# Kernel optimization log

Measured on AMD Instinct MI355X. Metric: run time of the kernel, lower is better.

The kernel has to match this reference:

```python
import jax, jax.numpy as jnp
import numpy as np

N_COMPONENTS = 64

def setup_inputs() -> dict:
    key = jax.random.key(0)
    x = jax.random.normal(key, (16, 128, 128, 128), dtype=jnp.float32)
    return {"x": x}

def reference(x):
    B = x.shape[0]
    C = x.shape[-1]
    flat = x.reshape(B, -1, C)                      # [B, N, C], N = H*W
    n = flat.shape[1]
    mean = jnp.mean(flat, axis=1, keepdims=True)    # [B, 1, C]
    centered = flat - mean                          # [B, N, C]
    cov = jnp.einsum('bnc,bnd->bcd', centered, centered) / jnp.float32(n - 1)  # [B, C, C]
    eigvals, eigvecs = jnp.linalg.eigh(cov)         # ascending eigenvalues
    idx = jnp.argsort(eigvals, axis=-1)[:, ::-1]    # descending order
    # gather eigenvector columns in descending-eigenvalue order
    top = jnp.take_along_axis(eigvecs, idx[:, None, :], axis=-1)[:, :, :N_COMPONENTS]  # [B, C, K]
    projected = jnp.einsum('bnc,bck->bnk', centered, top)  # [B, N, K]
    return projected.reshape(x.shape[:-1] + (N_COMPONENTS,))
```

## Files before the change

kernel.cpp:

```cpp
#include <hip/hip_runtime.h>

#define NC 128
#define KTOP 64
#define SMLSIZ 25
#define EPSF 5.9604645e-8f
#define SAFMINF 1.17549435e-38f
#define LDQ 129
#define THREADS 512

#define TBASEF 15400960
#define F_A    0
#define F_B    262144
#define F_Q    524288
#define F_Q2   786432
#define F_SM   1052672
#define F_VECS 1314816


__device__ __forceinline__ float slapy2f(float x, float y) {
  float xa = fabsf(x), ya = fabsf(y);
  float w = fmaxf(xa, ya), z = fminf(xa, ya);
  if (z == 0.f) return w;
  float r = z / w;
  return w * sqrtf(1.f + r * r);
}

__device__ __forceinline__ void slartgf(float f, float g, float* c, float* s, float* r) {
  if (g == 0.f) { *c = 1.f; *s = 0.f; *r = f; }
  else if (f == 0.f) { *c = 0.f; *s = (g >= 0.f) ? 1.f : -1.f; *r = fabsf(g); }
  else {
    float d_ = sqrtf(f * f + g * g);
    *c = fabsf(f) / d_;
    *r = (f >= 0.f) ? d_ : -d_;
    *s = g / (*r);
  }
}

__device__ void slaev2f(float a, float b, float c,
                        float* rt1, float* rt2, float* cs1, float* sn1) {
  float sm = a + c, df = a - c, adf = fabsf(df), tb = b + b, ab = fabsf(tb);
  float acmx, acmn;
  if (fabsf(a) > fabsf(c)) { acmx = a; acmn = c; } else { acmx = c; acmn = a; }
  float rt;
  if (adf > ab) { float t = ab / adf; rt = adf * sqrtf(1.f + t * t); }
  else if (adf < ab) { float t = adf / ab; rt = ab * sqrtf(1.f + t * t); }
  else rt = ab * sqrtf(2.f);
  int sgn1;
  if (sm < 0.f) { *rt1 = 0.5f * (sm - rt); sgn1 = -1; *rt2 = (acmx / (*rt1)) * acmn - (b / (*rt1)) * b; }
  else if (sm > 0.f) { *rt1 = 0.5f * (sm + rt); sgn1 = 1; *rt2 = (acmx / (*rt1)) * acmn - (b / (*rt1)) * b; }
  else { *rt1 = 0.5f * rt; *rt2 = -0.5f * rt; sgn1 = 1; }
  float cs; int sgn2;
  if (df >= 0.f) { cs = df + rt; sgn2 = 1; } else { cs = df - rt; sgn2 = -1; }
  float acs = fabsf(cs);
  if (acs > ab) {
    float ct = -tb / cs;
    *sn1 = 1.f / sqrtf(1.f + ct * ct);
    *cs1 = ct * (*sn1);
  } else {
    if (ab == 0.f) { *cs1 = 1.f; *sn1 = 0.f; }
    else { float tn = -cs / tb; *cs1 = 1.f / sqrtf(1.f + tn * tn); *sn1 = tn * (*cs1); }
  }
  if (sgn1 == sgn2) { float tn = *cs1; *cs1 = -(*sn1); *sn1 = tn; }
}

#define SDD(i) __shfl(dr, (i))
#define SEE(i) __shfl(er, (i))
__device__ void steqr_reg(float* d, float* e, int n, float* zb, int ldz, int lane) {
  const float eps = EPSF;
  const float eps2 = eps * eps;
  const float safmin = SAFMINF;
  for (int j = 0; j < n; j++)
    for (int i = lane; i < n; i += 64) zb[j * ldz + i] = (i == j) ? 1.f : 0.f;
  if (n <= 1) return;
  float dr = (lane < n) ? d[lane] : 0.f;
  float er = (lane < n - 1) ? e[lane] : 0.f;
  float cwr = 0.f, swr = 0.f;
  int nmaxit = n * 30, jtot = 0;
  int l1 = 1;
  while (true) {
    if (l1 > n) break;
    if (l1 > 1) er = (lane == l1 - 2) ? 0.f : er;
    int m;
    {
      int mm_;
      for (mm_ = l1; mm_ <= n - 1; mm_++) {
        float tst = fabsf(SEE(mm_ - 1));
        if (tst == 0.f) break;
        if (tst <= (sqrtf(fabsf(SDD(mm_ - 1))) * sqrtf(fabsf(SDD(mm_)))) * eps) {
          er = (lane == mm_ - 1) ? 0.f : er;
          break;
        }
      }
      m = mm_;
    }
    int l = l1, lsv = l, lend = m, lendsv = lend;
    l1 = m + 1;
    if (lend == l) continue;
    float anorm = 0.f;
    for (int i = l; i <= lend; i++) anorm = fmaxf(anorm, fabsf(SDD(i - 1)));
    for (int i = l; i <= lend - 1; i++) anorm = fmaxf(anorm, fabsf(SEE(i - 1)));
    if (anorm == 0.f) continue;
    if (fabsf(SDD(lend - 1)) < fabsf(SDD(l - 1))) { lend = lsv; l = lendsv; }
    if (lend > l) {
      while (true) {
        int m2;
        {
          int i;
          for (i = l; i <= lend - 1; i++) {
            float tst = fabsf(SEE(i - 1)); tst = tst * tst;
            if (tst <= (eps2 * fabsf(SDD(i - 1))) * fabsf(SDD(i)) + safmin) break;
          }
          m2 = i;
        }
        if (m2 < lend) er = (lane == m2 - 1) ? 0.f : er;
        float p = SDD(l - 1);
        if (m2 == l) { dr = (lane == l - 1) ? p : dr; l++; if (l <= lend) continue; else break; }
        if (m2 == l + 1) {
          float rt1, rt2, c_, s_;
          slaev2f(SDD(l - 1), SEE(l - 1), SDD(l), &rt1, &rt2, &c_, &s_);
          for (int i = lane; i < n; i += 64) {
            float t1 = zb[l * ldz + i];
            float t0 = zb[(l - 1) * ldz + i];
            zb[l * ldz + i] = c_ * t1 - s_ * t0;
            zb[(l - 1) * ldz + i] = s_ * t1 + c_ * t0;
          }
          dr = (lane == l - 1) ? rt1 : dr;
          dr = (lane == l) ? rt2 : dr;
          er = (lane == l - 1) ? 0.f : er;
          l += 2; if (l <= lend) continue; else break;
        }
        if (jtot == nmaxit) break;
        jtot++;
        float g = (SDD(l) - p) / (2.f * SEE(l - 1));
        float r = slapy2f(g, 1.f);
        g = SDD(m2 - 1) - p + SEE(l - 1) / (g + copysignf(r, g));
        float s_ = 1.f, c_ = 1.f; p = 0.f;
        for (int i = m2 - 1; i >= l; i--) {
          float ee = SEE(i - 1);
          float f = s_ * ee, b2 = c_ * ee;
          float cc, ss, rr;
          slartgf(g, f, &cc, &ss, &rr);
          c_ = cc; s_ = ss;
          if (i != m2 - 1) er = (lane == i) ? rr : er;
          g = SDD(i) - p;
          rr = (SDD(i - 1) - g) * s_ + 2.f * c_ * b2;
          p = s_ * rr;
          dr = (lane == i) ? (g + p) : dr;
          g = c_ * rr - b2;
          cwr = (lane == (i - l)) ? c_ : cwr;
          swr = (lane == (i - l)) ? (-s_) : swr;
        }
        int mm2 = m2 - l + 1;
        for (int jj = mm2 - 2; jj >= 0; jj--) {
          float ct_ = __shfl(cwr, jj), st_ = __shfl(swr, jj);
          int colj = l - 1 + jj;
          for (int i = lane; i < n; i += 64) {
            float t1 = zb[(colj + 1) * ldz + i];
            float t0 = zb[colj * ldz + i];
            zb[(colj + 1) * ldz + i] = ct_ * t1 - st_ * t0;
            zb[colj * ldz + i] = st_ * t1 + ct_ * t0;
          }
        }
        {
          float nv = SDD(l - 1) - p;
          dr = (lane == l - 1) ? nv : dr;
          er = (lane == l - 1) ? g : er;
        }
      }
    } else {
      while (true) {
        int m2;
        {
          int i;
          for (i = l; i >= lend + 1; i--) {
            float tst = fabsf(SEE(i - 2)); tst = tst * tst;
            if (tst <= (eps2 * fabsf(SDD(i - 1))) * fabsf(SDD(i - 2)) + safmin) break;
          }
          m2 = i;
        }
        if (m2 > lend) er = (lane == m2 - 2) ? 0.f : er;
        float p = SDD(l - 1);
        if (m2 == l) { dr = (lane == l - 1) ? p : dr; l--; if (l >= lend) continue; else break; }
        if (m2 == l - 1) {
          float rt1, rt2, c_, s_;
          slaev2f(SDD(l - 2), SEE(l - 2), SDD(l - 1), &rt1, &rt2, &c_, &s_);
          for (int i = lane; i < n; i += 64) {
            float t1 = zb[(l - 1) * ldz + i];
            float t0 = zb[(l - 2) * ldz + i];
            zb[(l - 1) * ldz + i] = c_ * t1 - s_ * t0;
            zb[(l - 2) * ldz + i] = s_ * t1 + c_ * t0;
          }
          dr = (lane == l - 2) ? rt1 : dr;
          dr = (lane == l - 1) ? rt2 : dr;
          er = (lane == l - 2) ? 0.f : er;
          l -= 2; if (l >= lend) continue; else break;
        }
        if (jtot == nmaxit) break;
        jtot++;
        float g = (SDD(l - 2) - p) / (2.f * SEE(l - 2));
        float r = slapy2f(g, 1.f);
        g = SDD(m2 - 1) - p + SEE(l - 2) / (g + copysignf(r, g));
        float s_ = 1.f, c_ = 1.f; p = 0.f;
        for (int i = m2; i <= l - 1; i++) {
          float ee = SEE(i - 1);
          float f = s_ * ee, b2 = c_ * ee;
          float cc, ss, rr;
          slartgf(g, f, &cc, &ss, &rr);
          c_ = cc; s_ = ss;
          if (i != m2) er = (lane == i - 2) ? rr : er;
          g = SDD(i - 1) - p;
          rr = (SDD(i) - g) * s_ + 2.f * c_ * b2;
          p = s_ * rr;
          dr = (lane == i - 1) ? (g + p) : dr;
          g = c_ * rr - b2;
          cwr = (lane == (i - m2)) ? c_ : cwr;
          swr = (lane == (i - m2)) ? s_ : swr;
        }
        int mm2 = l - m2 + 1;
        for (int jj = 0; jj <= mm2 - 2; jj++) {
          float ct_ = __shfl(cwr, jj), st_ = __shfl(swr, jj);
          int colj = m2 - 1 + jj;
          for (int i = lane; i < n; i += 64) {
            float t1 = zb[(colj + 1) * ldz + i];
            float t0 = zb[colj * ldz + i];
            zb[(colj + 1) * ldz + i] = ct_ * t1 - st_ * t0;
            zb[colj * ldz + i] = st_ * t1 + ct_ * t0;
          }
        }
        {
          float nv = SDD(l - 1) - p;
          dr = (lane == l - 1) ? nv : dr;
          er = (lane == l - 2) ? g : er;
        }
      }
    }
  }
  for (int ii = 2; ii <= n; ii++) {
    int i = ii - 1, k = i;
    float p = SDD(i - 1);
    for (int j = ii; j <= n; j++) {
      float dj = SDD(j - 1);
      if (dj < p) { k = j; p = dj; }
    }
    if (k != i) {
      float old = SDD(i - 1);
      dr = (lane == k - 1) ? old : dr;
      dr = (lane == i - 1) ? p : dr;
      for (int r = lane; r < n; r += 64) {
        float t5 = zb[(i - 1) * ldz + r];
        zb[(i - 1) * ldz + r] = zb[(k - 1) * ldz + r];
        zb[(k - 1) * ldz + r] = t5;
      }
    }
  }
  if (lane < n) d[lane] = dr;
  if (lane < n - 1) e[lane] = er;
}


__device__ void laed1_multi(float* d, float* e, float* Qm, float* Q2b, float* Smb,
                            float* zv, float* dl, float* wv, float* wg, float* pvf,
                            float* dvf, int* srcx, int* dsrc, int* iq,
                            int goff, const int* iwps, int p0, int G,
                            int tid, int* shi, float* shdf,
                            double* sdl, double* spv, int* defcnt) {
  int Tg = THREADS / G;
  int g = tid / Tg, gtid = tid - g * Tg;
  int pg = 2 * (p0 + g);
  int prev = (pg == 0) ? 0 : iwps[pg - 1];
  int off = goff + prev;
  int n = iwps[pg + 1] - prev;
  int n1 = (pg == 0) ? iwps[0] : (n / 2);
  int n2 = n - n1;
  float rho_in = e[off + n1 - 1];
  float* dg = d + off;
  float* zvg = zv + off;  float* dlg = dl + off;  float* wvg = wv + off;
  float* wgg = wg + off;  float* pvfg = pvf + off; float* dvfg = dvf + off;
  int* srcxg = srcx + off; int* dsrcg = dsrc + off; int* iqg = iq + off;
  double* sdlg = sdl + off; double* spvg = spv + off;
  float* Q2g = Q2b + (size_t)off * 128;
  float* Smg = Smb + (size_t)off * 128 + off;

  for (int t = gtid; t < n1; t += Tg) zvg[t] = Qm[(off + t) * LDQ + off + n1 - 1];
  for (int t = gtid; t < n2; t += Tg) zvg[n1 + t] = Qm[(off + n1 + t) * LDQ + off + n1];
  __syncthreads();
  if (gtid == 0) {
    float rho = rho_in;
    if (rho < 0.f) for (int t = n1; t < n; t++) zvg[t] = -zvg[t];
    float tsc = 1.0f / sqrtf(2.0f);
    for (int t = 0; t < n; t++) zvg[t] *= tsc;
    rho = fabsf(2.0f * rho);
    {
      int i = 0, j = n1, p = 0;
      while (i < n1 && j < n) {
        if (dg[i] <= dg[j]) srcxg[p++] = i++; else srcxg[p++] = j++;
      }
      while (i < n1) srcxg[p++] = i++;
      while (j < n) srcxg[p++] = j++;
    }
    int imax = 0, jmax = 0;
    for (int t = 1; t < n; t++) if (fabsf(zvg[t]) > fabsf(zvg[imax])) imax = t;
    for (int t = 1; t < n; t++) if (fabsf(dg[t]) > fabsf(dg[jmax])) jmax = t;
    float tol = 8.0f * EPSF * fmaxf(fabsf(dg[jmax]), fabsf(zvg[imax]));
    int k = 0, nd = 0;
    if (rho * fabsf(zvg[imax]) <= tol) {
      for (int t = 0; t < n; t++) { dsrcg[nd] = srcxg[t]; dvfg[nd] = dg[srcxg[t]]; nd++; }
    } else {
      int pj = -1;
      for (int jj = 0; jj < n; jj++) {
        int nj = srcxg[jj];
        if (rho * fabsf(zvg[nj]) <= tol) {
          dsrcg[nd] = nj; dvfg[nd] = dg[nj]; nd++;
        } else if (pj < 0) {
          pj = nj;
        } else {
          float s_ = zvg[pj], c_ = zvg[nj];
          float tau_ = slapy2f(c_, s_);
          float t3 = dg[nj] - dg[pj];
          c_ /= tau_; s_ = -s_ / tau_;
          if (fabsf(t3 * c_ * s_) <= tol) {
            zvg[nj] = tau_; zvg[pj] = 0.f;
            for (int r = 0; r < n; r++) {
              float x_ = Qm[(off + pj) * LDQ + off + r];
              float y_ = Qm[(off + nj) * LDQ + off + r];
              Qm[(off + pj) * LDQ + off + r] = c_ * x_ + s_ * y_;
              Qm[(off + nj) * LDQ + off + r] = c_ * y_ - s_ * x_;
            }
            float dp = dg[pj], dn = dg[nj];
            dg[nj] = dp * s_ * s_ + dn * c_ * c_;
            dg[pj] = dp * c_ * c_ + dn * s_ * s_;
            dsrcg[nd] = pj; dvfg[nd] = dg[pj]; nd++;
            pj = nj;
          } else {
            dlg[k] = dg[pj]; wvg[k] = zvg[pj]; srcxg[k] = pj; k++;
            pj = nj;
          }
        }
      }
      if (pj >= 0) { dlg[k] = dg[pj]; wvg[k] = zvg[pj]; srcxg[k] = pj; k++; }
    }
    shi[200 + g] = k; shi[208 + g] = nd; shdf[8 + g] = rho;
    if (nd > 0) atomicAdd(defcnt, nd);
  }
  __syncthreads();
  int k = shi[200 + g], nd = shi[208 + g];
  float rho = shdf[8 + g];
  if (k > 1) {
    for (int t = gtid; t < k; t += Tg) {
      sdlg[t] = (double)dlg[t];
      spvg[t] = (double)rho * (double)wvg[t] * (double)wvg[t];
    }
  }
  __syncthreads();
  if (k > 1 && gtid < k) {
    int j = gtid;
    double lo = 0.0, hi;
    if (j == k - 1) {
      double sw2 = 0.0;
      for (int t = 0; t < k; t++) sw2 += spvg[t];
      hi = sw2;
      for (int g2 = 0; g2 < 8; g2++) {
        double f = 1.0;
        for (int t = 0; t < k; t++) f += spvg[t] / ((sdlg[t] - sdlg[j]) - hi);
        if (f >= 0.0) break;
        hi *= 2.0;
      }
    } else hi = sdlg[j + 1] - sdlg[j];
    double gap = hi;
    double x = 0.5 * (lo + hi);
    for (int it = 0; it < 60; it++) {
      double f = 1.0, fp = 0.0;
      for (int t = 0; t < k; t++) {
        double inv = 1.0 / ((sdlg[t] - sdlg[j]) - x);
        double u = spvg[t] * inv;
        f += u; fp += u * inv;
      }
      if (f < 0.0) lo = x; else hi = x;
      double xn = x - f / fp;
      if (!(xn > lo && xn < hi)) xn = 0.5 * (lo + hi);
      if (xn == x) break;
      x = xn;
    }
    double eta = x;
    if (eta <= 0.0) eta = gap * 1e-30;
    if (j < k - 1 && eta >= gap) eta = gap * (1.0 - 1e-15);
    dg[j] = (float)(sdlg[j] + eta);
    for (int t = 0; t < k; t++)
      Smg[t * 128 + j] = (float)((sdlg[t] - sdlg[j]) - eta);
  }
  __syncthreads();
  if (k > 1 && gtid < k) {
    int i = gtid;
    float acc = Smg[i * 128 + i];
    for (int j = 0; j < k; j++) {
      if (j == i) continue;
      acc *= Smg[i * 128 + j] / (dlg[i] - dlg[j]);
    }
    wgg[i] = copysignf(sqrtf(fmaxf(-acc, 0.f)), wvg[i]);
  }
  __syncthreads();
  if (k > 1 && gtid < k) {
    int j = gtid;
    float nrm2 = 0.f;
    for (int i = 0; i < k; i++) {
      float u = wgg[i] / Smg[i * 128 + j];
      Smg[i * 128 + j] = u;
      nrm2 += u * u;
    }
    float nrm = sqrtf(nrm2);
    for (int i = 0; i < k; i++) Smg[i * 128 + j] /= nrm;
  }
  __syncthreads();
  if (k > 1) {
    int j = gtid & 127, rg = gtid >> 7;
    int RG = Tg >> 7; if (RG < 1) RG = 1;
    if (j < k) {
      int chunk = (n + RG - 1) / RG;
      int rbeg = rg * chunk, rend = rbeg + chunk;
      if (rend > n) rend = n;
      int r0 = rbeg;
      for (; r0 + 8 <= rend; r0 += 8) {
        float a0 = 0.f, a1 = 0.f, a2 = 0.f, a3 = 0.f;
        float a4 = 0.f, a5 = 0.f, a6 = 0.f, a7 = 0.f;
        for (int i = 0; i < k; i++) {
          float s = Smg[i * 128 + j];
          const float* q = &Qm[(off + srcxg[i]) * LDQ + off + r0];
          a0 += q[0] * s; a1 += q[1] * s; a2 += q[2] * s; a3 += q[3] * s;
          a4 += q[4] * s; a5 += q[5] * s; a6 += q[6] * s; a7 += q[7] * s;
        }
        float* o = &Q2g[j * 128 + r0];
        o[0] = a0; o[1] = a1; o[2] = a2; o[3] = a3;
        o[4] = a4; o[5] = a5; o[6] = a6; o[7] = a7;
      }
      for (; r0 < rend; r0++) {
        float a = 0.f;
        for (int i = 0; i < k; i++)
          a += Qm[(off + srcxg[i]) * LDQ + off + r0] * Smg[i * 128 + j];
        Q2g[j * 128 + r0] = a;
      }
    }
  } else if (k == 1 && gtid == 0) {
    zvg[0] = dlg[0] + rho * (wvg[0] * wvg[0]);
    for (int r = 0; r < n; r++) Q2g[r] = Qm[(off + srcxg[0]) * LDQ + off + r];
  }
  __syncthreads();
  if (k > 1 && gtid < k) zvg[gtid] = dg[gtid];
  __syncthreads();
  for (int t2 = gtid; t2 < nd; t2 += Tg)
    for (int r = 0; r < n; r++) Q2g[(k + t2) * 128 + r] = Qm[(off + dsrcg[t2]) * LDQ + off + r];
  for (int j = gtid; j < n; j += Tg) pvfg[j] = (j < k) ? zvg[j] : dvfg[j - k];
  __syncthreads();
  for (int j = gtid; j < n; j += Tg) {
    float kj = pvfg[j];
    int r = 0;
    for (int i = 0; i < n; i++) {
      float ki = pvfg[i];
      if (ki < kj || (ki == kj && i < j)) r++;
    }
    iqg[r] = j;
  }
  __syncthreads();
  {
    int j = gtid & 127, rg = gtid >> 7;
    int RG = Tg >> 7; if (RG < 1) RG = 1;
    if (j < n) {
      int s2 = iqg[j];
      if (rg == 0) dg[j] = pvfg[s2];
      int chunk = (n + RG - 1) / RG;
      int rbeg = rg * chunk, rend = rbeg + chunk;
      if (rend > n) rend = n;
      for (int r = rbeg; r < rend; r++) Qm[(off + j) * LDQ + off + r] = Q2g[s2 * 128 + r];
    }
  }
  __syncthreads();
}

__device__ void laed0_f32(float* d, float* e, float* Qm, float* Q2, float* Sm,
                          float* zv, float* dl, float* wv, float* wg, float* pvf,
                          float* dvf, int* srcx, int* dsrc, int* iq, int* iwps,
                          int goff, int m, int tid, int* shi, float* shdf,
                          double* sdl, double* spv, int* defcnt) {
  if (tid == 0) {
    iwps[0] = m; int sp = 1;
    while (iwps[sp - 1] > SMLSIZ) {
      for (int j = sp - 1; j >= 0; j--) { iwps[2 * j + 1] = (iwps[j] + 1) / 2; iwps[2 * j] = iwps[j] / 2; }
      sp *= 2;
    }
    for (int j = 1; j < sp; j++) iwps[j] += iwps[j - 1];
    shi[134] = sp;
    for (int i = 0; i < sp - 1; i++) {
      int bnd = goff + iwps[i];
      d[bnd - 1] -= fabsf(e[bnd - 1]);
      d[bnd] -= fabsf(e[bnd - 1]);
    }
  }
  __syncthreads();
  int subpbs = shi[134];
  {
    int lw = tid >> 6;
    if (lw < subpbs) {
      int boff = goff + (lw == 0 ? 0 : iwps[lw - 1]);
      int bm = iwps[lw] - (lw == 0 ? 0 : iwps[lw - 1]);
      steqr_reg(d + boff, e + boff, bm, Qm + boff * LDQ + boff, LDQ, tid & 63);
    }
  }
  __syncthreads();
  int cur = subpbs;
  while (cur > 1) {
    int nm = cur >> 1;
    for (int p0 = 0; p0 < nm; ) {
      int G = (nm - p0 >= 4) ? 4 : ((nm - p0 >= 2) ? 2 : 1);
      laed1_multi(d, e, Qm, Q2, Sm, zv, dl, wv, wg, pvf, dvf, srcx, dsrc, iq,
                  goff, iwps, p0, G, tid, shi, shdf, sdl, spv, defcnt);
      p0 += G;
    }
    if (tid == 0) for (int t = 0; 2 * t + 1 < cur; t++) iwps[t] = iwps[2 * t + 1];
    __syncthreads();
    cur >>= 1;
  }
}


__global__ __launch_bounds__(THREADS) void eig_p1_kernel(const float* __restrict__ covB,
                                                         float* __restrict__ Aout,
                                                         float* __restrict__ vecs) {
  int b = blockIdx.x, tid = threadIdx.x;
  const float* Cg = covB + (size_t)b * 16384;
  float* Ag = Aout + (size_t)b * 16384;
  __shared__ float As[16384];
  __shared__ float sh_e[128], sh_tau[128], sh_pvf[128];
  __shared__ float redf[128];
  __shared__ float shdf[4];
  float* A = As; float* e = sh_e; float* tauv = sh_tau; float* pvf = sh_pvf;

  for (int idx = tid; idx < 16384; idx += THREADS) As[idx] = Cg[idx];
  if (tid < 128) { sh_e[tid] = 0.f; sh_tau[tid] = 0.f; }
  __syncthreads();

  for (int i1 = 1; i1 <= NC - 1; i1++) {
    int ii = i1 - 1;
    int mlen = NC - i1;
    float ps = 0.f;
    if (tid < 128) {
      for (int t = tid; t < mlen - 1; t += 128) {
        float v = A[ii * 128 + ii + 2 + t];
        ps += v * v;
      }
      redf[tid] = ps;
    }
    __syncthreads();
    if (tid < 64) {
      float a = redf[tid] + redf[tid + 64];
      a += __shfl_xor(a, 32); a += __shfl_xor(a, 16); a += __shfl_xor(a, 8);
      a += __shfl_xor(a, 4);  a += __shfl_xor(a, 2);  a += __shfl_xor(a, 1);
      if (tid == 0) {
        float xnorm = sqrtf(a);
        float alpha = A[ii * 128 + ii + 1];
        float taui, ei, scl;
        if (xnorm == 0.f) { taui = 0.f; ei = alpha; scl = 0.f; }
        else {
          float beta = -copysignf(slapy2f(alpha, xnorm), alpha);
          taui = (beta - alpha) / beta;
          scl = 1.f / (alpha - beta);
          ei = beta;
        }
        e[ii] = ei; tauv[ii] = taui; shdf[2] = scl;
      }
    }
    __syncthreads();
    float taui = tauv[ii];
    if (taui != 0.f) {
      float scl = shdf[2];
      for (int t = tid; t < mlen - 1; t += 128) A[ii * 128 + ii + 2 + t] *= scl;
      __syncthreads();
      for (int r = tid; r < mlen; r += 128) {
        float acc = 0.f;
        int row = ii + 1 + r;
        acc += A[(ii + 1) * 128 + row];
        for (int s = 1; s < mlen; s++) acc += A[(ii + 1 + s) * 128 + row] * A[ii * 128 + ii + 1 + s];
        pvf[r] = taui * acc;
      }
      __syncthreads();
      if (tid < 128) {
        float pd = 0.f;
        for (int t = tid; t < mlen; t += 128) {
          float vt = (t == 0) ? 1.f : A[ii * 128 + ii + 1 + t];
          pd += pvf[t] * vt;
        }
        redf[tid] = pd;
      }
      __syncthreads();
      if (tid < 64) {
        float a = redf[tid] + redf[tid + 64];
        a += __shfl_xor(a, 32); a += __shfl_xor(a, 16); a += __shfl_xor(a, 8);
        a += __shfl_xor(a, 4);  a += __shfl_xor(a, 2);  a += __shfl_xor(a, 1);
        if (tid == 0) shdf[3] = -0.5f * taui * a;
      }
      __syncthreads();
      float alpha2 = shdf[3];
      for (int t = tid; t < mlen; t += 128) {
        float vt = (t == 0) ? 1.f : A[ii * 128 + ii + 1 + t];
        pvf[t] += alpha2 * vt;
      }
      __syncthreads();
      if ((tid & 127) < mlen) {
        int r = tid & 127, g = tid >> 7;
        int chunk = (mlen + 3) >> 2;
        int cb = g * chunk, ce = cb + chunk;
        if (ce > mlen) ce = mlen;
        float vr = (r == 0) ? 1.f : A[ii * 128 + ii + 1 + r];
        float pr = pvf[r];
        for (int c2 = cb; c2 < ce; c2++) {
          float vc = (c2 == 0) ? 1.f : A[ii * 128 + ii + 1 + c2];
          A[(ii + 1 + c2) * 128 + (ii + 1 + r)] -= vr * pvf[c2] + pr * vc;
        }
      }
      __syncthreads();
    }
  }
  for (int idx = tid; idx < 16384; idx += THREADS) Ag[idx] = As[idx];
  if (tid < 128) {
    vecs[b * 128 + tid] = As[tid * 128 + tid];
    vecs[2048 + b * 128 + tid] = sh_e[tid];
    vecs[4096 + b * 128 + tid] = sh_tau[tid];
  }
}


__global__ __launch_bounds__(THREADS) void eig_p2_kernel(float* __restrict__ Qw,
                                                         float* Q2w, float* Sw,
                                                         float* vecs, int* defcnt) {
  int b = blockIdx.x, tid = threadIdx.x;
  float* Qg = Qw + (size_t)b * 16384;
  float* Q2 = Q2w + (size_t)b * 16640;
  float* Sm = Sw + (size_t)b * 16384;

  __shared__ float Qs[128 * LDQ];
  __shared__ float sh_d[128], sh_e[128], sh_zv[128], sh_dl[128];
  __shared__ float sh_wv[128], sh_wg[128], sh_pvf[128], sh_dvf[128];
  __shared__ int sh_iq[128], sh_srcx[128], sh_dsrc[128];
  __shared__ int iwps[64];
  __shared__ float shdf[16];
  __shared__ int shi[280];
  __shared__ double sdl[128];
  __shared__ double spv[128];

  float* Qm = Qs;
  float* d = sh_d; float* e = sh_e; float* zv = sh_zv;
  float* dl = sh_dl; float* wv = sh_wv; float* wg = sh_wg; float* pvf = sh_pvf;
  float* dvf = sh_dvf;
  int* iq = sh_iq; int* srcx = sh_srcx; int* dsrc = sh_dsrc;

  if (tid < 128) {
    sh_d[tid] = vecs[b * 128 + tid];
    sh_e[tid] = vecs[2048 + b * 128 + tid];
  }
  for (int idx = tid; idx < 16384; idx += THREADS) {
    int c = idx >> 7, r = idx & 127;
    Qs[c * LDQ + r] = (c == r) ? 1.f : 0.f;
  }
  __syncthreads();
  if (tid == 0) {
    int ns = 0, start = 0;
    while (start < NC) {
      int fin = start;
      while (fin < NC - 1) {
        float tiny = EPSF * sqrtf(fabsf(d[fin])) * sqrtf(fabsf(d[fin + 1]));
        if (fabsf(e[fin]) > tiny) fin++;
        else break;
      }
      shi[2 + 2 * ns] = start; shi[3 + 2 * ns] = fin - start + 1; ns++;
      start = fin + 1;
    }
    shi[0] = ns;
  }
  __syncthreads();
  int nsplit = shi[0];
  for (int sb = 0; sb < nsplit; sb++) {
    int goff = shi[2 + 2 * sb], m = shi[3 + 2 * sb];
    if (m == 1) continue;
    if (m <= SMLSIZ) {
      if (tid < 64) steqr_reg(d + goff, e + goff, m, Qm + goff * LDQ + goff, LDQ, tid);
      __syncthreads();
    } else {
      if (tid == 0) {
        float mx = 0.f;
        for (int i = 0; i < m; i++) mx = fmaxf(mx, fabsf(d[goff + i]));
        for (int i = 0; i < m - 1; i++) mx = fmaxf(mx, fabsf(e[goff + i]));
        shdf[0] = mx;
      }
      __syncthreads();
      float onrm = shdf[0];
      if (onrm != 0.f) {
        float mul = 1.f / onrm;
        for (int t = tid; t < m; t += 128) d[goff + t] *= mul;
        for (int t = tid; t < m - 1; t += 128) e[goff + t] *= mul;
        __syncthreads();
        laed0_f32(d, e, Qm, Q2, Sm, zv, dl, wv, wg, pvf, dvf, srcx, dsrc, iq,
                  iwps, goff, m, tid, shi, shdf, sdl, spv, defcnt);
        for (int t = tid; t < m; t += 128) d[goff + t] *= onrm;
        __syncthreads();
      }
    }
  }
  if (tid < 128) {
    float kj = d[tid];
    int r = 0;
    for (int i = 0; i < 128; i++) {
      float ki = d[i];
      if (ki < kj || (ki == kj && i < tid)) r++;
    }
    shi[140 + r] = tid;
    zv[r] = kj;
  }
  __syncthreads();
  if (tid < 128) d[tid] = zv[tid];
  __syncthreads();
  {
    int j = tid & 127, g = tid >> 7;
    int rbeg = g * 32, rend = rbeg + 32;
    int src = shi[140 + j];
    for (int r = rbeg; r < rend; r++) Q2[j * 128 + r] = Qm[src * LDQ + r];
  }
  __syncthreads();
  {
    int j = tid & 127, g = tid >> 7;
    int rbeg = g * 32, rend = rbeg + 32;
    for (int r = rbeg; r < rend; r++) Qm[j * LDQ + r] = Q2[j * 128 + r];
  }
  __syncthreads();
  for (int idx = tid; idx < 16384; idx += THREADS) {
    int c = idx >> 7, r = idx & 127;
    Qg[idx] = Qs[c * LDQ + r];
  }
  if (tid < 128) vecs[b * 128 + tid] = d[tid];
}


__global__ __launch_bounds__(THREADS) void eig_p3_kernel(const float* __restrict__ Ain,
                                                         const float* __restrict__ vecs,
                                                         float* __restrict__ Qw,
                                                         float* __restrict__ Vw) {
  int b = blockIdx.x, tid = threadIdx.x;
  const float* Ag = Ain + (size_t)b * 16384;
  float* Qg = Qw + (size_t)b * 16384;
  __shared__ float As[16384];
  __shared__ float Qs[128 * LDQ];
  __shared__ float sh_tau[128];
  float* A = As; float* Qm = Qs; float* tauv = sh_tau;

  for (int idx = tid; idx < 16384; idx += THREADS) As[idx] = Ag[idx];
  for (int idx = tid; idx < 16384; idx += THREADS) {
    int c = idx >> 7, r = idx & 127;
    Qs[c * LDQ + r] = Qg[idx];
  }
  if (tid < 128) sh_tau[tid] = vecs[4096 + b * 128 + tid];
  __syncthreads();

  for (int j1 = NC - 1; j1 >= 1; j1--) {
    int jj = j1 - 1;
    float tj = tauv[jj];
    if (tj != 0.f) {
      if (tid < NC) {
        int col = tid;
        float s = Qm[col * LDQ + jj + 1];
        for (int r = jj + 2; r < NC; r++) s += A[jj * 128 + r] * Qm[col * LDQ + r];
        s *= tj;
        Qm[col * LDQ + jj + 1] -= s;
        for (int r = jj + 2; r < NC; r++) Qm[col * LDQ + r] -= s * A[jj * 128 + r];
      }
    }
  }
  __syncthreads();

  for (int idx = tid; idx < NC * KTOP; idx += THREADS) {
    int c2 = idx / KTOP, kk = idx % KTOP;
    Vw[(size_t)b * (NC * KTOP) + idx] = Qm[(127 - kk) * LDQ + c2];
  }
  for (int idx = tid; idx < 16384; idx += THREADS) {
    int c = idx >> 7, r = idx & 127;
    Qg[idx] = Qs[c * LDQ + r];
  }
}


__global__ void zeroi_kernel(int* p) { p[0] = 0; p[1] = 0; }

__global__ __launch_bounds__(128) void diag_kernel(const float* __restrict__ covB,
                                                   const float* __restrict__ Qw,
                                                   const float* __restrict__ vecs,
                                                   const float* __restrict__ Vw, int* dcode) {
  int b = blockIdx.x, tid = threadIdx.x;
  const float* C = covB + (size_t)b * 16384;
  const float* Qm = Qw + (size_t)b * 16384;
  const float* d = vecs + b * 128;
  int flags = 0;
  double rmax = 0.0;
  for (int k = 64; k < 128; k++) {
    double lam = (double)d[k];
    double acc = 0.0;
    for (int j = 0; j < 128; j++) acc += (double)C[j * 128 + tid] * (double)Qm[k * 128 + j];
    acc -= lam * (double)Qm[k * 128 + tid];
    rmax = fmax(rmax, fabs(acc));
  }
  if (rmax > 1e-3) flags |= 1;
  double omax = 0.0;
  for (int p = tid; p < 64 * 64; p += 128) {
    int i = 64 + p / 64, j = 64 + p % 64;
    if (j < i) continue;
    double s = 0.0;
    for (int r = 0; r < 128; r++) s += (double)Qm[i * 128 + r] * (double)Qm[j * 128 + r];
    if (i == j) s -= 1.0;
    omax = fmax(omax, fabs(s));
  }
  if (omax > 1e-3) flags |= 2;
  if (tid < 127 && d[tid + 1] < d[tid] - 1e-5f) flags |= 4;
  for (int idx = tid; idx < 8192; idx += 128) {
    int c2 = idx / 64, kk = idx % 64;
    if (Vw[(size_t)b * 8192 + idx] != Qm[(127 - kk) * 128 + c2]) flags |= 8;
  }
  if (tid == 0) {
    for (int k = 64; k < 128; k++) if (!(d[k] > 0.2f && d[k] < 5.0f)) flags |= 16;
    float s = 0.f;
    for (int c = 0; c < 128; c++) { float v = Vw[(size_t)b * 8192 + c * 64]; s += v * v; }
    if (fabsf(s - 1.f) > 1e-2f) flags |= 32;
  }
  if (flags) atomicOr(dcode, flags);
}

__global__ void emit_kernel(const int* dcode, float* out) {
  int f = dcode[0];
  if (f) {
    int code = 1000;
    if (f & 1) code += 400;
    if (f & 2) code += 200;
    if (f & 4) code += 100;
    if (f & 8) code += 40;
    if (f & 16) code += 20;
    if (f & 32) code += 10;
    int nd = dcode[1]; if (nd > 9) nd = 9;
    code += nd;
    out[0] = (float)code;
  }
}


__global__ __launch_bounds__(128) void mean_np_kernel(const float* __restrict__ x,
                                                      float* __restrict__ mean32) {
  int b = blockIdx.x, c = threadIdx.x;
  const float* xb = x + (size_t)b * 2097152;
  float s = 0.0f;
#pragma unroll 16
  for (int n = 0; n < 16384; n++) s = __fadd_rn(s, xb[n * 128 + c]);
  mean32[b * 128 + c] = s / 16384.0f;
}

__global__ __launch_bounds__(256) void covnp_kernel(const float* __restrict__ x,
                                                    const float* __restrict__ mean32,
                                                    float* __restrict__ S) {
  int b = blockIdx.x;
  int p = blockIdx.y;
  int ti4, tj4;
  if (p < 4) { ti4 = 0; tj4 = p; }
  else if (p < 7) { ti4 = 1; tj4 = p - 3; }
  else if (p < 9) { ti4 = 2; tj4 = p - 5; }
  else { ti4 = 3; tj4 = 3; }
  int ti = ti4 * 32, tj = tj4 * 32;
  __shared__ float XI[32 * 66], XJ[32 * 66];
  int tid = threadIdx.x;
  int ci = 2 * (tid & 15), dj = 2 * (tid >> 4);
  float a00 = 0.f, a01 = 0.f, a10 = 0.f, a11 = 0.f;
  const float* xb = x + (size_t)b * 2097152;
  const float* mb = mean32 + b * 128;
  for (int n0 = 0; n0 < 16384; n0 += 64) {
    __syncthreads();
    for (int l = tid; l < 2048; l += 256) {
      int n = l >> 5, cc = l & 31;
      XI[cc * 66 + n] = __fsub_rn(xb[(n0 + n) * 128 + ti + cc], mb[ti + cc]);
      XJ[cc * 66 + n] = __fsub_rn(xb[(n0 + n) * 128 + tj + cc], mb[tj + cc]);
    }
    __syncthreads();
    const float2* pi0 = (const float2*)&XI[ci * 66];
    const float2* pi1 = (const float2*)&XI[(ci + 1) * 66];
    const float2* pj0 = (const float2*)&XJ[dj * 66];
    const float2* pj1 = (const float2*)&XJ[(dj + 1) * 66];
    for (int n2 = 0; n2 < 32; n2++) {
      float2 xi0 = pi0[n2], xi1 = pi1[n2], xj0 = pj0[n2], xj1 = pj1[n2];
      a00 = __fadd_rn(a00, __fmul_rn(xi0.x, xj0.x));
      a01 = __fadd_rn(a01, __fmul_rn(xi0.x, xj1.x));
      a10 = __fadd_rn(a10, __fmul_rn(xi1.x, xj0.x));
      a11 = __fadd_rn(a11, __fmul_rn(xi1.x, xj1.x));
      a00 = __fadd_rn(a00, __fmul_rn(xi0.y, xj0.y));
      a01 = __fadd_rn(a01, __fmul_rn(xi0.y, xj1.y));
      a10 = __fadd_rn(a10, __fmul_rn(xi1.y, xj0.y));
      a11 = __fadd_rn(a11, __fmul_rn(xi1.y, xj1.y));
    }
  }
  float* Sb = S + (size_t)b * 16384;
  int C = ti + ci, D = tj + dj;
  Sb[C * 128 + D] = a00;
  Sb[C * 128 + D + 1] = a01;
  Sb[(C + 1) * 128 + D] = a10;
  Sb[(C + 1) * 128 + D + 1] = a11;
}

__global__ void covfin_kernel(const float* __restrict__ A, float* __restrict__ B) {
  int i = blockIdx.x * 256 + threadIdx.x;
  if (i < 262144) {
    int w = i & 16383;
    int base = i - w;
    int r = w >> 7, c = w & 127;
    int src = ((r >> 5) > (c >> 5)) ? (base + c * 128 + r) : i;
    B[i] = A[src] / 16383.0f;
  }
}


__global__ __launch_bounds__(256) void proj_kernel(const float* __restrict__ x, const float* __restrict__ V,
                                                   const float* __restrict__ mean32, float* __restrict__ out) {
  __shared__ float Vs[128 * 64];
  __shared__ float Xs[64 * 128];
  __shared__ float ms[128];
  int b = blockIdx.x, t = blockIdx.y, tid = threadIdx.x;
  const float* xb = x + (size_t)b * 2097152 + (size_t)t * 64 * 128;
  const float* vb = V + (size_t)b * 8192;
  if (tid < 128) ms[tid] = mean32[b * 128 + tid];
  __syncthreads();
  for (int i = tid; i < 2048; i += 256) ((float4*)Vs)[i] = ((const float4*)vb)[i];
  for (int i = tid; i < 2048; i += 256) {
    float4 xv = ((const float4*)xb)[i];
    int cv = (i & 31) * 4;
    xv.x -= ms[cv]; xv.y -= ms[cv + 1]; xv.z -= ms[cv + 2]; xv.w -= ms[cv + 3];
    ((float4*)Xs)[i] = xv;
  }
  __syncthreads();
  int kk = tid & 63, w = tid >> 6;
  float acc[16];
#pragma unroll
  for (int r = 0; r < 16; r++) acc[r] = 0.f;
  for (int c4 = 0; c4 < 32; c4++) {
    float v0 = Vs[(c4 * 4 + 0) * 64 + kk];
    float v1 = Vs[(c4 * 4 + 1) * 64 + kk];
    float v2 = Vs[(c4 * 4 + 2) * 64 + kk];
    float v3 = Vs[(c4 * 4 + 3) * 64 + kk];
#pragma unroll
    for (int r = 0; r < 16; r++) {
      const float4 xv = ((const float4*)Xs)[(w * 16 + r) * 32 + c4];
      acc[r] += xv.x * v0 + xv.y * v1 + xv.z * v2 + xv.w * v3;
    }
  }
  float* ob = out + (size_t)b * 1048576 + (size_t)t * 4096;
#pragma unroll
  for (int r = 0; r < 16; r++) ob[(w * 16 + r) * 64 + kk] = acc[r];
}


extern "C" void kernel_launch(void* const* d_in, const int* in_sizes, int n_in,
                              void* d_out, int out_size, void* d_ws, size_t ws_size,
                              hipStream_t stream) {
  (void)in_sizes; (void)n_in; (void)out_size; (void)ws_size;
  const float* x = (const float*)d_in[0];
  float* out = (float*)d_out;
  float* T = out + TBASEF;
  float* Af   = T + F_A;
  float* Bf   = T + F_B;
  float* Qf   = T + F_Q;
  float* Q2f  = T + F_Q2;
  float* Smf  = T + F_SM;
  float* vecsf = T + F_VECS;
  float* Vw = (float*)d_ws;
  float* mean32 = Vw + 131072;
  int* dcode = (int*)(mean32 + 2048);

  zeroi_kernel<<<dim3(1), dim3(1), 0, stream>>>(dcode);
  mean_np_kernel<<<dim3(16), dim3(128), 0, stream>>>(x, mean32);
  covnp_kernel<<<dim3(16, 10), dim3(256), 0, stream>>>(x, mean32, Af);
  covfin_kernel<<<dim3(1024), dim3(256), 0, stream>>>(Af, Bf);
  eig_p1_kernel<<<dim3(16), dim3(THREADS), 0, stream>>>(Bf, Af, vecsf);
  eig_p2_kernel<<<dim3(16), dim3(THREADS), 0, stream>>>(Qf, Q2f, Smf, vecsf, dcode + 1);
  eig_p3_kernel<<<dim3(16), dim3(THREADS), 0, stream>>>(Af, vecsf, Qf, Vw);
  diag_kernel<<<dim3(16), dim3(128), 0, stream>>>(Bf, Qf, vecsf, Vw, dcode);
  proj_kernel<<<dim3(16, 256), dim3(256), 0, stream>>>(x, Vw, mean32, out);
  emit_kernel<<<dim3(1), dim3(1), 0, stream>>>(dcode, out);
}
```

Before: 4.776 ms.

## Split eigen merge into three kernels and keep secular matrix in LDS

The divide-and-conquer eigensolver stage is split into three launches: leaf QR solves, all merges except the last, and the final merge plus sort. Split metadata and norms are passed through the vecs workspace. The secular-equation matrix Sm moves from global memory to a padded LDS array (stride 129), removing global round-trips in the merge's inner loops. The cost is extra launches, Q reloads and stores between stages, and higher per-block LDS use. The mean kernel's unroll factor also rises from 16 to 64.

```diff
diff --git a/kernel.cpp b/kernel.cpp
--- a/kernel.cpp
+++ b/kernel.cpp
@@ -6,6 +6,7 @@
 #define EPSF 5.9604645e-8f
 #define SAFMINF 1.17549435e-38f
 #define LDQ 129
+#define LDS_SM 129
 #define THREADS 512
 
 #define TBASEF 15400960
@@ -13,7 +14,6 @@
 #define F_B    262144
 #define F_Q    524288
 #define F_Q2   786432
-#define F_SM   1052672
 #define F_VECS 1314816
 
 
@@ -279,7 +279,7 @@
   int* srcxg = srcx + off; int* dsrcg = dsrc + off; int* iqg = iq + off;
   double* sdlg = sdl + off; double* spvg = spv + off;
   float* Q2g = Q2b + (size_t)off * 128;
-  float* Smg = Smb + (size_t)off * 128 + off;
+  float* Smg = Smb + (size_t)off * LDS_SM + off;
 
   for (int t = gtid; t < n1; t += Tg) zvg[t] = Qm[(off + t) * LDQ + off + n1 - 1];
   for (int t = gtid; t < n2; t += Tg) zvg[n1 + t] = Qm[(off + n1 + t) * LDQ + off + n1];
@@ -386,15 +386,15 @@
     if (j < k - 1 && eta >= gap) eta = gap * (1.0 - 1e-15);
     dg[j] = (float)(sdlg[j] + eta);
     for (int t = 0; t < k; t++)
-      Smg[t * 128 + j] = (float)((sdlg[t] - sdlg[j]) - eta);
+      Smg[t * LDS_SM + j] = (float)((sdlg[t] - sdlg[j]) - eta);
   }
   __syncthreads();
   if (k > 1 && gtid < k) {
     int i = gtid;
-    float acc = Smg[i * 128 + i];
+    float acc = Smg[i * LDS_SM + i];
     for (int j = 0; j < k; j++) {
       if (j == i) continue;
-      acc *= Smg[i * 128 + j] / (dlg[i] - dlg[j]);
+      acc *= Smg[i * LDS_SM + j] / (dlg[i] - dlg[j]);
     }
     wgg[i] = copysignf(sqrtf(fmaxf(-acc, 0.f)), wvg[i]);
   }
@@ -403,12 +403,12 @@
     int j = gtid;
     float nrm2 = 0.f;
     for (int i = 0; i < k; i++) {
-      float u = wgg[i] / Smg[i * 128 + j];
-      Smg[i * 128 + j] = u;
+      float u = wgg[i] / Smg[i * LDS_SM + j];
+      Smg[i * LDS_SM + j] = u;
       nrm2 += u * u;
     }
     float nrm = sqrtf(nrm2);
-    for (int i = 0; i < k; i++) Smg[i * 128 + j] /= nrm;
+    for (int i = 0; i < k; i++) Smg[i * LDS_SM + j] /= nrm;
   }
   __syncthreads();
   if (k > 1) {
@@ -423,7 +423,7 @@
         float a0 = 0.f, a1 = 0.f, a2 = 0.f, a3 = 0.f;
         float a4 = 0.f, a5 = 0.f, a6 = 0.f, a7 = 0.f;
         for (int i = 0; i < k; i++) {
-          float s = Smg[i * 128 + j];
+          float s = Smg[i * LDS_SM + j];
           const float* q = &Qm[(off + srcxg[i]) * LDQ + off + r0];
           a0 += q[0] * s; a1 += q[1] * s; a2 += q[2] * s; a3 += q[3] * s;
           a4 += q[4] * s; a5 += q[5] * s; a6 += q[6] * s; a7 += q[7] * s;
@@ -435,7 +435,7 @@
       for (; r0 < rend; r0++) {
         float a = 0.f;
         for (int i = 0; i < k; i++)
-          a += Qm[(off + srcxg[i]) * LDQ + off + r0] * Smg[i * 128 + j];
+          a += Qm[(off + srcxg[i]) * LDQ + off + r0] * Smg[i * LDS_SM + j];
         Q2g[j * 128 + r0] = a;
       }
     }
@@ -473,51 +473,6 @@
     }
   }
   __syncthreads();
-}
-
-__device__ void laed0_f32(float* d, float* e, float* Qm, float* Q2, float* Sm,
-                          float* zv, float* dl, float* wv, float* wg, float* pvf,
-                          float* dvf, int* srcx, int* dsrc, int* iq, int* iwps,
-                          int goff, int m, int tid, int* shi, float* shdf,
-                          double* sdl, double* spv, int* defcnt) {
-  if (tid == 0) {
-    iwps[0] = m; int sp = 1;
-    while (iwps[sp - 1] > SMLSIZ) {
-      for (int j = sp - 1; j >= 0; j--) { iwps[2 * j + 1] = (iwps[j] + 1) / 2; iwps[2 * j] = iwps[j] / 2; }
-      sp *= 2;
-    }
-    for (int j = 1; j < sp; j++) iwps[j] += iwps[j - 1];
-    shi[134] = sp;
-    for (int i = 0; i < sp - 1; i++) {
-      int bnd = goff + iwps[i];
-      d[bnd - 1] -= fabsf(e[bnd - 1]);
-      d[bnd] -= fabsf(e[bnd - 1]);
-    }
-  }
-  __syncthreads();
-  int subpbs = shi[134];
-  {
-    int lw = tid >> 6;
-    if (lw < subpbs) {
-      int boff = goff + (lw == 0 ? 0 : iwps[lw - 1]);
-      int bm = iwps[lw] - (lw == 0 ? 0 : iwps[lw - 1]);
-      steqr_reg(d + boff, e + boff, bm, Qm + boff * LDQ + boff, LDQ, tid & 63);
-    }
-  }
-  __syncthreads();
-  int cur = subpbs;
-  while (cur > 1) {
-    int nm = cur >> 1;
-    for (int p0 = 0; p0 < nm; ) {
-      int G = (nm - p0 >= 4) ? 4 : ((nm - p0 >= 2) ? 2 : 1);
-      laed1_multi(d, e, Qm, Q2, Sm, zv, dl, wv, wg, pvf, dvf, srcx, dsrc, iq,
-                  goff, iwps, p0, G, tid, shi, shdf, sdl, spv, defcnt);
-      p0 += G;
-    }
-    if (tid == 0) for (int t = 0; 2 * t + 1 < cur; t++) iwps[t] = iwps[2 * t + 1];
-    __syncthreads();
-    cur >>= 1;
-  }
 }
 
 
@@ -627,15 +582,108 @@
 }
 
 
-__global__ __launch_bounds__(THREADS) void eig_p2_kernel(float* __restrict__ Qw,
-                                                         float* Q2w, float* Sw,
-                                                         float* vecs, int* defcnt) {
+__global__ __launch_bounds__(THREADS) void eig_p2a_kernel(float* __restrict__ Qw,
+                                                          float* __restrict__ vecs) {
+  int b = blockIdx.x, tid = threadIdx.x;
+  float* Qg = Qw + (size_t)b * 16384;
+  __shared__ float Qs[128 * LDQ];
+  __shared__ float sh_d[128], sh_e[128];
+  __shared__ int iwps[64];
+  __shared__ float shdf[16];
+  __shared__ int shi[280];
+  float* Qm = Qs; float* d = sh_d; float* e = sh_e;
+  int* meta = (int*)(vecs + 6144) + b * 320;
+  float* onrmv = vecs + 11264 + b * 128;
+
+  if (tid < 128) { sh_d[tid] = vecs[b * 128 + tid]; sh_e[tid] = vecs[2048 + b * 128 + tid]; }
+  for (int idx = tid; idx < 16384; idx += THREADS) {
+    int c = idx >> 7, r = idx & 127;
+    Qs[c * LDQ + r] = (c == r) ? 1.f : 0.f;
+  }
+  __syncthreads();
+  if (tid == 0) {
+    int ns = 0, start = 0;
+    while (start < NC) {
+      int fin = start;
+      while (fin < NC - 1) {
+        float tiny = EPSF * sqrtf(fabsf(d[fin])) * sqrtf(fabsf(d[fin + 1]));
+        if (fabsf(e[fin]) > tiny) fin++;
+        else break;
+      }
+      shi[2 + 2 * ns] = start; shi[3 + 2 * ns] = fin - start + 1; ns++;
+      start = fin + 1;
+    }
+    shi[0] = ns;
+    meta[0] = ns;
+    for (int s = 0; s < ns; s++) { meta[1 + 2 * s] = shi[2 + 2 * s]; meta[2 + 2 * s] = shi[3 + 2 * s]; }
+  }
+  __syncthreads();
+  int nsplit = shi[0];
+  for (int sb = 0; sb < nsplit; sb++) {
+    int goff = shi[2 + 2 * sb], m = shi[3 + 2 * sb];
+    if (m == 1) { if (tid == 0) onrmv[sb] = 0.f; continue; }
+    if (m <= SMLSIZ) {
+      if (tid == 0) onrmv[sb] = 0.f;
+      if (tid < 64) steqr_reg(d + goff, e + goff, m, Qm + goff * LDQ + goff, LDQ, tid);
+      __syncthreads();
+    } else {
+      if (tid == 0) {
+        float mx = 0.f;
+        for (int i = 0; i < m; i++) mx = fmaxf(mx, fabsf(d[goff + i]));
+        for (int i = 0; i < m - 1; i++) mx = fmaxf(mx, fabsf(e[goff + i]));
+        shdf[0] = mx;
+        onrmv[sb] = mx;
+      }
+      __syncthreads();
+      float onrm = shdf[0];
+      if (onrm != 0.f) {
+        float mul = 1.f / onrm;
+        for (int t = tid; t < m; t += 128) d[goff + t] *= mul;
+        for (int t = tid; t < m - 1; t += 128) e[goff + t] *= mul;
+        __syncthreads();
+        if (tid == 0) {
+          iwps[0] = m; int sp = 1;
+          while (iwps[sp - 1] > SMLSIZ) {
+            for (int j = sp - 1; j >= 0; j--) { iwps[2 * j + 1] = (iwps[j] + 1) / 2; iwps[2 * j] = iwps[j] / 2; }
+            sp *= 2;
+          }
+          for (int j = 1; j < sp; j++) iwps[j] += iwps[j - 1];
+          shi[134] = sp;
+          for (int i = 0; i < sp - 1; i++) {
+            int bnd = goff + iwps[i];
+            d[bnd - 1] -= fabsf(e[bnd - 1]);
+            d[bnd] -= fabsf(e[bnd - 1]);
+          }
+        }
+        __syncthreads();
+        int subpbs = shi[134];
+        {
+          int lw = tid >> 6;
+          if (lw < subpbs) {
+            int boff = goff + (lw == 0 ? 0 : iwps[lw - 1]);
+            int bm = iwps[lw] - (lw == 0 ? 0 : iwps[lw - 1]);
+            steqr_reg(d + boff, e + boff, bm, Qm + boff * LDQ + boff, LDQ, tid & 63);
+          }
+        }
+        __syncthreads();
+      }
+    }
+  }
+  if (tid < 128) { vecs[b * 128 + tid] = sh_d[tid]; vecs[2048 + b * 128 + tid] = sh_e[tid]; }
+  for (int idx = tid; idx < 16384; idx += THREADS) {
+    int c = idx >> 7, r = idx & 127;
+    Qg[idx] = Qs[c * LDQ + r];
+  }
+}
+
+
+__global__ __launch_bounds__(THREADS) void eig_p2b_kernel(float* __restrict__ Qw,
+                                                          float* Q2w, float* vecs, int* defcnt) {
   int b = blockIdx.x, tid = threadIdx.x;
   float* Qg = Qw + (size_t)b * 16384;
   float* Q2 = Q2w + (size_t)b * 16640;
-  float* Sm = Sw + (size_t)b * 16384;
-
   __shared__ float Qs[128 * LDQ];
+  __shared__ float Sms[128 * LDS_SM];
   __shared__ float sh_d[128], sh_e[128], sh_zv[128], sh_dl[128];
   __shared__ float sh_wv[128], sh_wg[128], sh_pvf[128], sh_dvf[128];
   __shared__ int sh_iq[128], sh_srcx[128], sh_dsrc[128];
@@ -644,64 +692,103 @@
   __shared__ int shi[280];
   __shared__ double sdl[128];
   __shared__ double spv[128];
-
   float* Qm = Qs;
-  float* d = sh_d; float* e = sh_e; float* zv = sh_zv;
-  float* dl = sh_dl; float* wv = sh_wv; float* wg = sh_wg; float* pvf = sh_pvf;
-  float* dvf = sh_dvf;
-  int* iq = sh_iq; int* srcx = sh_srcx; int* dsrc = sh_dsrc;
-
-  if (tid < 128) {
-    sh_d[tid] = vecs[b * 128 + tid];
-    sh_e[tid] = vecs[2048 + b * 128 + tid];
-  }
+  int* meta = (int*)(vecs + 6144) + b * 320;
+  float* onrmv = vecs + 11264 + b * 128;
+
+  if (tid < 128) { sh_d[tid] = vecs[b * 128 + tid]; sh_e[tid] = vecs[2048 + b * 128 + tid]; }
   for (int idx = tid; idx < 16384; idx += THREADS) {
     int c = idx >> 7, r = idx & 127;
-    Qs[c * LDQ + r] = (c == r) ? 1.f : 0.f;
-  }
-  __syncthreads();
-  if (tid == 0) {
-    int ns = 0, start = 0;
-    while (start < NC) {
-      int fin = start;
-      while (fin < NC - 1) {
-        float tiny = EPSF * sqrtf(fabsf(d[fin])) * sqrtf(fabsf(d[fin + 1]));
-        if (fabsf(e[fin]) > tiny) fin++;
-        else break;
-      }
-      shi[2 + 2 * ns] = start; shi[3 + 2 * ns] = fin - start + 1; ns++;
-      start = fin + 1;
-    }
-    shi[0] = ns;
-  }
-  __syncthreads();
-  int nsplit = shi[0];
+    Qs[c * LDQ + r] = Qg[idx];
+  }
+  __syncthreads();
+  int nsplit = meta[0];
   for (int sb = 0; sb < nsplit; sb++) {
-    int goff = shi[2 + 2 * sb], m = shi[3 + 2 * sb];
-    if (m == 1) continue;
-    if (m <= SMLSIZ) {
-      if (tid < 64) steqr_reg(d + goff, e + goff, m, Qm + goff * LDQ + goff, LDQ, tid);
+    int goff = meta[1 + 2 * sb], m = meta[2 + 2 * sb];
+    float onrm = onrmv[sb];
+    if (onrm == 0.f || m <= SMLSIZ) continue;
+    if (tid == 0) {
+      iwps[0] = m; int sp = 1;
+      while (iwps[sp - 1] > SMLSIZ) {
+        for (int j = sp - 1; j >= 0; j--) { iwps[2 * j + 1] = (iwps[j] + 1) / 2; iwps[2 * j] = iwps[j] / 2; }
+        sp *= 2;
+      }
+      for (int j = 1; j < sp; j++) iwps[j] += iwps[j - 1];
+      shi[134] = sp;
+    }
+    __syncthreads();
+    int cur = shi[134];
+    while (cur > 2) {
+      int nm = cur >> 1;
+      for (int p0 = 0; p0 < nm; ) {
+        int G = (nm - p0 >= 4) ? 4 : ((nm - p0 >= 2) ? 2 : 1);
+        laed1_multi(sh_d, sh_e, Qm, Q2, Sms, sh_zv, sh_dl, sh_wv, sh_wg, sh_pvf, sh_dvf,
+                    sh_srcx, sh_dsrc, sh_iq, goff, iwps, p0, G, tid, shi, shdf, sdl, spv, defcnt);
+        p0 += G;
+      }
+      if (tid == 0) for (int t = 0; 2 * t + 1 < cur; t++) iwps[t] = iwps[2 * t + 1];
       __syncthreads();
-    } else {
-      if (tid == 0) {
-        float mx = 0.f;
-        for (int i = 0; i < m; i++) mx = fmaxf(mx, fabsf(d[goff + i]));
-        for (int i = 0; i < m - 1; i++) mx = fmaxf(mx, fabsf(e[goff + i]));
-        shdf[0] = mx;
-      }
+      cur >>= 1;
+    }
+  }
+  if (tid < 128) vecs[b * 128 + tid] = sh_d[tid];
+  for (int idx = tid; idx < 16384; idx += THREADS) {
+    int c = idx >> 7, r = idx & 127;
+    Qg[idx] = Qs[c * LDQ + r];
+  }
+}
+
+
+__global__ __launch_bounds__(THREADS) void eig_p2c_kernel(float* __restrict__ Qw,
+                                                          float* Q2w, float* vecs, int* defcnt) {
+  int b = blockIdx.x, tid = threadIdx.x;
+  float* Qg = Qw + (size_t)b * 16384;
+  float* Q2 = Q2w + (size_t)b * 16640;
+  __shared__ float Qs[128 * LDQ];
+  __shared__ float Sms[128 * LDS_SM];
+  __shared__ float sh_d[128], sh_e[128], sh_zv[128], sh_dl[128];
+  __shared__ float sh_wv[128], sh_wg[128], sh_pvf[128], sh_dvf[128];
+  __shared__ int sh_iq[128], sh_srcx[128], sh_dsrc[128];
+  __shared__ int iwps[64];
+  __shared__ float shdf[16];
+  __shared__ int shi[280];
+  __shared__ double sdl[128];
+  __shared__ double spv[128];
+  float* Qm = Qs; float* d = sh_d; float* zv = sh_zv;
+  int* meta = (int*)(vecs + 6144) + b * 320;
+  float* onrmv = vecs + 11264 + b * 128;
+
+  if (tid < 128) { sh_d[tid] = vecs[b * 128 + tid]; sh_e[tid] = vecs[2048 + b * 128 + tid]; }
+  for (int idx = tid; idx < 16384; idx += THREADS) {
+    int c = idx >> 7, r = idx & 127;
+    Qs[c * LDQ + r] = Qg[idx];
+  }
+  __syncthreads();
+  int nsplit = meta[0];
+  for (int sb = 0; sb < nsplit; sb++) {
+    int goff = meta[1 + 2 * sb], m = meta[2 + 2 * sb];
+    float onrm = onrmv[sb];
+    if (onrm == 0.f || m <= SMLSIZ) continue;
+    if (tid == 0) {
+      iwps[0] = m; int sp = 1;
+      while (iwps[sp - 1] > SMLSIZ) {
+        for (int j = sp - 1; j >= 0; j--) { iwps[2 * j + 1] = (iwps[j] + 1) / 2; iwps[2 * j] = iwps[j] / 2; }
+        sp *= 2;
+      }
+      for (int j = 1; j < sp; j++) iwps[j] += iwps[j - 1];
+      shi[134] = sp;
+    }
+    __syncthreads();
+    int cur = shi[134];
+    while (cur > 2) {
+      if (tid == 0) for (int t = 0; 2 * t + 1 < cur; t++) iwps[t] = iwps[2 * t + 1];
       __syncthreads();
-      float onrm = shdf[0];
-      if (onrm != 0.f) {
-        float mul = 1.f / onrm;
-        for (int t = tid; t < m; t += 128) d[goff + t] *= mul;
-        for (int t = tid; t < m - 1; t += 128) e[goff + t] *= mul;
-        __syncthreads();
-        laed0_f32(d, e, Qm, Q2, Sm, zv, dl, wv, wg, pvf, dvf, srcx, dsrc, iq,
-                  iwps, goff, m, tid, shi, shdf, sdl, spv, defcnt);
-        for (int t = tid; t < m; t += 128) d[goff + t] *= onrm;
-        __syncthreads();
-      }
-    }
+      cur >>= 1;
+    }
+    laed1_multi(sh_d, sh_e, Qm, Q2, Sms, sh_zv, sh_dl, sh_wv, sh_wg, sh_pvf, sh_dvf,
+                sh_srcx, sh_dsrc, sh_iq, goff, iwps, 0, 1, tid, shi, shdf, sdl, spv, defcnt);
+    for (int t = tid; t < m; t += 128) d[goff + t] *= onrm;
+    __syncthreads();
   }
   if (tid < 128) {
     float kj = d[tid];
@@ -850,7 +937,7 @@
   int b = blockIdx.x, c = threadIdx.x;
   const float* xb = x + (size_t)b * 2097152;
   float s = 0.0f;
-#pragma unroll 16
+#pragma unroll 64
   for (int n = 0; n < 16384; n++) s = __fadd_rn(s, xb[n * 128 + c]);
   mean32[b * 128 + c] = s / 16384.0f;
 }
@@ -966,7 +1053,6 @@
   float* Bf   = T + F_B;
   float* Qf   = T + F_Q;
   float* Q2f  = T + F_Q2;
-  float* Smf  = T + F_SM;
   float* vecsf = T + F_VECS;
   float* Vw = (float*)d_ws;
   float* mean32 = Vw + 131072;
@@ -977,7 +1063,9 @@
   covnp_kernel<<<dim3(16, 10), dim3(256), 0, stream>>>(x, mean32, Af);
   covfin_kernel<<<dim3(1024), dim3(256), 0, stream>>>(Af, Bf);
   eig_p1_kernel<<<dim3(16), dim3(THREADS), 0, stream>>>(Bf, Af, vecsf);
-  eig_p2_kernel<<<dim3(16), dim3(THREADS), 0, stream>>>(Qf, Q2f, Smf, vecsf, dcode + 1);
+  eig_p2a_kernel<<<dim3(16), dim3(THREADS), 0, stream>>>(Qf, vecsf);
+  eig_p2b_kernel<<<dim3(16), dim3(THREADS), 0, stream>>>(Qf, Q2f, vecsf, dcode + 1);
+  eig_p2c_kernel<<<dim3(16), dim3(THREADS), 0, stream>>>(Qf, Q2f, vecsf, dcode + 1);
   eig_p3_kernel<<<dim3(16), dim3(THREADS), 0, stream>>>(Af, vecsf, Qf, Vw);
   diag_kernel<<<dim3(16), dim3(128), 0, stream>>>(Bf, Qf, vecsf, Vw, dcode);
   proj_kernel<<<dim3(16, 256), dim3(256), 0, stream>>>(x, Vw, mean32, out);
```

Result: faster. 4.437 ms (-7.1%).
